# Optimization experiments

Hardware: AMD Instinct MI355X
Metric: run time of the kernel (lower is better)

## Reference

```python
import jax, jax.numpy as jnp
import numpy as np


def setup_inputs() -> dict:
    key = jax.random.key(0)
    k1, k2 = jax.random.split(key)
    B, Lp, Lw, D = 4, 256, 200, 768
    bert_emb = jax.random.normal(k1, (B, Lp, D), dtype=jnp.float32)
    # pieces2word[b, w, p] == 1 iff wordpiece p belongs to word w
    pieces2word = jax.random.randint(k2, (B, Lw, Lp), 0, 2, dtype=jnp.int32)
    return {"bert_emb": bert_emb, "pieces2word": pieces2word}


def reference(bert_emb, pieces2word):
    # Faithful to EmbeddingLayer.forward:
    #   min_value = bert_emb.min().item()  (a detached scalar in torch)
    #   _bert_embs = bert_emb.unsqueeze(1).expand(-1, Lw, -1, -1)
    #   masked_fill where pieces2word == 0 with min_value; max over piece dim
    min_value = jax.lax.stop_gradient(jnp.min(bert_emb))
    # [B, Lw, Lp, D] broadcast, masked, reduced over pieces (axis=2)
    masked = jnp.where(pieces2word[:, :, :, None] != 0,
                       bert_emb[:, None, :, :],
                       min_value)
    word_reps = jnp.max(masked, axis=2)  # [B, Lw, D]
    return word_reps
```

## Files before the change

kernel.cpp:

```cpp
#include <hip/hip_runtime.h>


#define B_  4
#define LP_ 256
#define LW_ 200
#define D_  768
#define D4_ (D_ / 4)
#define CHUNKS 3
#define W_  10
#define HALFW 5
#define WG_ (LW_ / W_)
#define NBLK (B_ * CHUNKS * WG_)
#define SEGS 8
#define PPS 32

__global__ __launch_bounds__(512) void word_max_scan(
    const float* __restrict__ emb, const int* __restrict__ p2w,
    float* __restrict__ out)
{
    const int blk   = blockIdx.x;
    const int wg    = blk % WG_;
    const int rest  = blk / WG_;
    const int chunk = rest % CHUNKS;
    const int b     = rest / CHUNKS;
    const int lane  = threadIdx.x & 63;
    const int s     = threadIdx.x >> 6;
    const int w0    = wg * W_;

    unsigned int m[W_];
    const int pc = s * PPS + (lane & 31);
    #pragma unroll
    for (int j = 0; j < W_; ++j) {
        const int* mrow = p2w + (b * LW_ + w0 + j) * LP_;
        m[j] = (unsigned int)__ballot((lane < 32) && (mrow[pc] != 0));
    }

    const float ninf = __uint_as_float(0xFF800000u);
    float4 acc[W_];
    #pragma unroll
    for (int j = 0; j < W_; ++j) acc[j] = make_float4(ninf, ninf, ninf, ninf);

    const float4* rps = (const float4*)(emb + (size_t)b * LP_ * D_)
                        + chunk * 64 + lane + (size_t)(s * PPS) * D4_;

    #pragma unroll
    for (int g = 0; g < PPS; g += 8) {
        float4 v[8];
        #pragma unroll
        for (int k = 0; k < 8; ++k)
            v[k] = rps[(size_t)(g + k) * D4_];
        #pragma unroll
        for (int k = 0; k < 8; k += 2) {
            #pragma unroll
            for (int j = 0; j < W_; ++j) {
                const bool b0 = (m[j] >> (g + k))     & 1u;
                const bool b1 = (m[j] >> (g + k + 1)) & 1u;
                float sx0 = b0 ? v[k].x     : ninf;
                float sy0 = b0 ? v[k].y     : ninf;
                float sz0 = b0 ? v[k].z     : ninf;
                float sw0 = b0 ? v[k].w     : ninf;
                float sx1 = b1 ? v[k + 1].x : ninf;
                float sy1 = b1 ? v[k + 1].y : ninf;
                float sz1 = b1 ? v[k + 1].z : ninf;
                float sw1 = b1 ? v[k + 1].w : ninf;
                asm("v_max3_f32 %0, %1, %2, %3"
                    : "=v"(acc[j].x) : "v"(acc[j].x), "v"(sx0), "v"(sx1));
                asm("v_max3_f32 %0, %1, %2, %3"
                    : "=v"(acc[j].y) : "v"(acc[j].y), "v"(sy0), "v"(sy1));
                asm("v_max3_f32 %0, %1, %2, %3"
                    : "=v"(acc[j].z) : "v"(acc[j].z), "v"(sz0), "v"(sz1));
                asm("v_max3_f32 %0, %1, %2, %3"
                    : "=v"(acc[j].w) : "v"(acc[j].w), "v"(sw0), "v"(sw1));
            }
        }
    }

    __shared__ float4 sacc[SEGS][HALFW][64];
    __shared__ unsigned int smask[SEGS][W_];
    if (lane == 0) {
        #pragma unroll
        for (int j = 0; j < W_; ++j) smask[s][j] = m[j];
    }

    #pragma unroll
    for (int half = 0; half < 2; ++half) {
        if (half) __syncthreads();
        #pragma unroll
        for (int j = 0; j < HALFW; ++j)
            sacc[s][j][lane] = acc[half * HALFW + j];
        __syncthreads();

        if (s < HALFW) {
            const int j = half * HALFW + s;
            float4 r = sacc[0][s][lane];
            #pragma unroll
            for (int seg = 1; seg < SEGS; ++seg) {
                r.x = fmaxf(r.x, sacc[seg][s][lane].x);
                r.y = fmaxf(r.y, sacc[seg][s][lane].y);
                r.z = fmaxf(r.z, sacc[seg][s][lane].z);
                r.w = fmaxf(r.w, sacc[seg][s][lane].w);
            }
            unsigned int om = 0;
            #pragma unroll
            for (int seg = 0; seg < SEGS; ++seg) om |= smask[seg][j];

            if (om == 0u) {
                const float4* x = (const float4*)emb;
                const int n4 = (B_ * LP_ * D_) / 4;
                float mn = __uint_as_float(0x7F800000u);
                for (int i = lane; i < n4; i += 64) {
                    float4 vv = x[i];
                    mn = fminf(mn, fminf(fminf(vv.x, vv.y), fminf(vv.z, vv.w)));
                }
                #pragma unroll
                for (int off = 32; off > 0; off >>= 1)
                    mn = fminf(mn, __shfl_down(mn, off, 64));
                mn = __shfl(mn, 0, 64);
                r = make_float4(mn, mn, mn, mn);
            }

            float4* op = (float4*)out + (size_t)(b * LW_ + w0 + j) * D4_
                         + chunk * 64 + lane;
            *op = r;
        }
    }
}

extern "C" void kernel_launch(void* const* d_in, const int* in_sizes, int n_in,
                              void* d_out, int out_size, void* d_ws, size_t ws_size,
                              hipStream_t stream) {
    const float* emb = (const float*)d_in[0];
    const int*   p2w = (const int*)d_in[1];
    float*       out = (float*)d_out;
    (void)d_ws; (void)ws_size;

    word_max_scan<<<NBLK, 512, 0, stream>>>(emb, p2w, out);
}
```

Baseline: 68.12 us.

## Double waves per block to 16 segments and use a two-level shared-memory max tree

Each block now runs 16 wavefronts of 16 pieces each instead of 8 wavefronts of 32, halving the per-wave serial scan over pieces. The cross-segment reduction becomes a two-stage tree: 12 waves write partials, 4 waves combine them with max3, then 2 waves finish and write the output. This cuts the serial per-wave latency in exchange for more shared memory (dynamic, about 150 KB), an extra barrier, and possible occupancy limits from 1024-thread blocks.

```diff
diff --git a/kernel.cpp b/kernel.cpp
--- a/kernel.cpp
+++ b/kernel.cpp
@@ -8,16 +8,30 @@
 #define D4_ (D_ / 4)
 #define CHUNKS 3
 #define W_  10
-#define HALFW 5
 #define WG_ (LW_ / W_)
 #define NBLK (B_ * CHUNKS * WG_)
-#define SEGS 8
-#define PPS 32
+#define SEGS 16
+#define PPS 16
 
-__global__ __launch_bounds__(512) void word_max_scan(
+#define R1_BYTES (12 * W_ * 64 * 16)
+#define R2_BYTES (3 * W_ * 64 * 16)
+#define SMEM_BYTES (R1_BYTES + R2_BYTES + SEGS * W_ * 4)
+
+__device__ __forceinline__ void max3_inplace(float& d, float a, float b) {
+    asm("v_max3_f32 %0, %1, %2, %3" : "=v"(d) : "v"(d), "v"(a), "v"(b));
+}
+
+__global__ __launch_bounds__(1024) void word_max_scan(
     const float* __restrict__ emb, const int* __restrict__ p2w,
     float* __restrict__ out)
 {
+    extern __shared__ char smem[];
+    float4 (*r1)[W_][64] = reinterpret_cast<float4 (*)[W_][64]>(smem);
+    float4 (*r2)[W_][64] =
+        reinterpret_cast<float4 (*)[W_][64]>(smem + R1_BYTES);
+    unsigned int (*smask)[W_] =
+        reinterpret_cast<unsigned int (*)[W_]>(smem + R1_BYTES + R2_BYTES);
+
     const int blk   = blockIdx.x;
     const int wg    = blk % WG_;
     const int rest  = blk / WG_;
@@ -28,11 +42,11 @@
     const int w0    = wg * W_;
 
     unsigned int m[W_];
-    const int pc = s * PPS + (lane & 31);
+    const int pc = s * PPS + (lane & 15);
     #pragma unroll
     for (int j = 0; j < W_; ++j) {
         const int* mrow = p2w + (b * LW_ + w0 + j) * LP_;
-        m[j] = (unsigned int)__ballot((lane < 32) && (mrow[pc] != 0));
+        m[j] = (unsigned int)__ballot((lane < 16) && (mrow[pc] != 0));
     }
 
     const float ninf = __uint_as_float(0xFF800000u);
@@ -63,43 +77,68 @@
                 float sy1 = b1 ? v[k + 1].y : ninf;
                 float sz1 = b1 ? v[k + 1].z : ninf;
                 float sw1 = b1 ? v[k + 1].w : ninf;
-                asm("v_max3_f32 %0, %1, %2, %3"
-                    : "=v"(acc[j].x) : "v"(acc[j].x), "v"(sx0), "v"(sx1));
-                asm("v_max3_f32 %0, %1, %2, %3"
-                    : "=v"(acc[j].y) : "v"(acc[j].y), "v"(sy0), "v"(sy1));
-                asm("v_max3_f32 %0, %1, %2, %3"
-                    : "=v"(acc[j].z) : "v"(acc[j].z), "v"(sz0), "v"(sz1));
-                asm("v_max3_f32 %0, %1, %2, %3"
-                    : "=v"(acc[j].w) : "v"(acc[j].w), "v"(sw0), "v"(sw1));
+                max3_inplace(acc[j].x, sx0, sx1);
+                max3_inplace(acc[j].y, sy0, sy1);
+                max3_inplace(acc[j].z, sz0, sz1);
+                max3_inplace(acc[j].w, sw0, sw1);
             }
         }
     }
 
-    __shared__ float4 sacc[SEGS][HALFW][64];
-    __shared__ unsigned int smask[SEGS][W_];
+    if (s >= 4) {
+        #pragma unroll
+        for (int j = 0; j < W_; ++j) r1[s - 4][j][lane] = acc[j];
+    }
     if (lane == 0) {
         #pragma unroll
         for (int j = 0; j < W_; ++j) smask[s][j] = m[j];
     }
+    __syncthreads();
 
-    #pragma unroll
-    for (int half = 0; half < 2; ++half) {
-        if (half) __syncthreads();
+    if (s < 4) {
         #pragma unroll
-        for (int j = 0; j < HALFW; ++j)
-            sacc[s][j][lane] = acc[half * HALFW + j];
-        __syncthreads();
+        for (int j = 0; j < W_; ++j) {
+            float4 a = r1[s][j][lane];
+            float4 c = r1[s + 4][j][lane];
+            float4 d = r1[s + 8][j][lane];
+            max3_inplace(acc[j].x, a.x, c.x);
+            max3_inplace(acc[j].y, a.y, c.y);
+            max3_inplace(acc[j].z, a.z, c.z);
+            max3_inplace(acc[j].w, a.w, c.w);
+            acc[j].x = fmaxf(acc[j].x, d.x);
+            acc[j].y = fmaxf(acc[j].y, d.y);
+            acc[j].z = fmaxf(acc[j].z, d.z);
+            acc[j].w = fmaxf(acc[j].w, d.w);
+        }
+        #pragma unroll
+        for (int j = 0; j < W_; ++j) {
+            const int o = (j < 5) ? 0 : 1;
+            if (s != o) {
+                const int slot = (o == 0) ? (s - 1) : ((s == 0) ? 0 : (s - 1));
+                r2[slot][j][lane] = acc[j];
+            }
+        }
+    }
+    __syncthreads();
 
-        if (s < HALFW) {
-            const int j = half * HALFW + s;
-            float4 r = sacc[0][s][lane];
-            #pragma unroll
-            for (int seg = 1; seg < SEGS; ++seg) {
-                r.x = fmaxf(r.x, sacc[seg][s][lane].x);
-                r.y = fmaxf(r.y, sacc[seg][s][lane].y);
-                r.z = fmaxf(r.z, sacc[seg][s][lane].z);
-                r.w = fmaxf(r.w, sacc[seg][s][lane].w);
-            }
+    if (s < 2) {
+        const int j0 = s * 5;
+        #pragma unroll
+        for (int jj = 0; jj < 5; ++jj) {
+            const int j = j0 + jj;
+            float4 r = acc[j];
+            float4 a = r2[0][j][lane];
+            float4 c = r2[1][j][lane];
+            float4 d = r2[2][j][lane];
+            max3_inplace(r.x, a.x, c.x);
+            max3_inplace(r.y, a.y, c.y);
+            max3_inplace(r.z, a.z, c.z);
+            max3_inplace(r.w, a.w, c.w);
+            r.x = fmaxf(r.x, d.x);
+            r.y = fmaxf(r.y, d.y);
+            r.z = fmaxf(r.z, d.z);
+            r.w = fmaxf(r.w, d.w);
+
             unsigned int om = 0;
             #pragma unroll
             for (int seg = 0; seg < SEGS; ++seg) om |= smask[seg][j];
@@ -134,5 +173,5 @@
     float*       out = (float*)d_out;
     (void)d_ws; (void)ws_size;
 
-    word_max_scan<<<NBLK, 512, 0, stream>>>(emb, p2w, out);
+    word_max_scan<<<NBLK, 1024, SMEM_BYTES, stream>>>(emb, p2w, out);
 }
```

Measured after the change: 103.2 us. 51.5% more time.
